# Kernel tuning notes

Hardware: AMD Instinct MI355X
Metric: run time of the kernel (lower is better)

## Reference

```python
import jax, jax.numpy as jnp
import numpy as np

MAX_SEQ_LEN = 64
BEAM = 8
NEG_INF = -1e30


def gru_cell(x, h, W_ih, W_hh, b_ih, b_hh):
    # PyTorch GRUCell math. x: [N,E], h: [N,H]
    H = h.shape[-1]
    gi = x @ W_ih.T + b_ih  # [N,3H]
    gh = h @ W_hh.T + b_hh  # [N,3H]
    r = jax.nn.sigmoid(gi[:, :H] + gh[:, :H])
    z = jax.nn.sigmoid(gi[:, H:2 * H] + gh[:, H:2 * H])
    n = jnp.tanh(gi[:, 2 * H:] + r * gh[:, 2 * H:])
    return (1.0 - z) * n + z * h


def decoder_step(tok, h, embedding, W_ih, W_hh, b_ih, b_hh, W_out, b_out):
    emb = embedding[tok]                      # [N,E] gather
    h2 = gru_cell(emb, h, W_ih, W_hh, b_ih, b_hh)
    logits = h2 @ W_out.T + b_out             # [N,V]
    return logits, h2


def beam_search(encoded, embedding, W_ih, W_hh, b_ih, b_hh, W_out, b_out, bos_index, eos_index):
    B, H = encoded.shape
    V = embedding.shape[0]
    K, T = BEAM, MAX_SEQ_LEN
    dec = lambda tok, h: decoder_step(tok, h, embedding, W_ih, W_hh, b_ih, b_hh, W_out, b_out)

    # step 0: bos
    bos = jnp.full((B,), bos_index, jnp.int32)
    logits0, h0 = dec(bos, encoded)
    lp0 = jax.nn.log_softmax(logits0, axis=1)
    vals, idx = jax.lax.top_k(lp0, K)  # [B,K]
    lp_hist = jnp.zeros((B, K, T), jnp.float32).at[:, :, 0].set(vals)
    tok_hist = jnp.zeros((B, K, T), jnp.int32).at[:, :, 0].set(idx)
    last = idx.reshape(B * K)
    # hidden.repeat(1, K).view(B*K, H): tile each row K times
    hidden = jnp.broadcast_to(h0[:, None, :], (B, K, H)).reshape(B * K, H)
    is_eos = (jnp.arange(V) == eos_index)  # [V]

    def step(carry, t):
        last, hidden, prev_vals, prev_tok, lp_hist, tok_hist = carry
        logits, hidden = dec(last, hidden)
        lp = jax.nn.log_softmax(logits, axis=1).reshape(B, K, V)
        combined = prev_vals[:, :, None] + lp
        has_fin = (prev_tok == eos_index)[:, :, None]  # [B,K,1]
        masked = jnp.where(is_eos[None, None, :] & has_fin, 0.0, combined)
        masked = jnp.where((~is_eos)[None, None, :] & has_fin, NEG_INF, masked)
        vals, idx = jax.lax.top_k(masked.reshape(B, K * V), K)  # [B,K]
        tokens = idx % V
        which = idx // V
        hidden = jnp.take_along_axis(hidden.reshape(B, K, H), which[:, :, None], axis=1).reshape(B * K, H)
        lp_hist = jnp.take_along_axis(lp_hist, which[:, :, None], axis=1)
        tok_hist = jnp.take_along_axis(tok_hist, which[:, :, None], axis=1)
        lp_hist = jax.lax.dynamic_update_slice(lp_hist, vals[:, :, None], (0, 0, t))
        tok_hist = jax.lax.dynamic_update_slice(tok_hist, tokens[:, :, None], (0, 0, t))
        return (tokens.reshape(B * K), hidden, vals, tokens, lp_hist, tok_hist), None

    carry = (last, hidden, vals, idx, lp_hist, tok_hist)
    (last, hidden, vals, idx, lp_hist, tok_hist), _ = jax.lax.scan(step, carry, jnp.arange(1, T))
    return lp_hist, tok_hist


def setup_inputs() -> dict:
    key = jax.random.key(0)
    ks = jax.random.split(key, 8)
    B, V, E, H = 4, 32000, 512, 1024
    s = 0.05
    return {
        "encoded": jax.random.normal(ks[0], (B, H), jnp.float32),
        "embedding": jax.random.normal(ks[1], (V, E), jnp.float32) * s,
        "W_ih": jax.random.normal(ks[2], (3 * H, E), jnp.float32) * s,
        "W_hh": jax.random.normal(ks[3], (3 * H, H), jnp.float32) * s,
        "b_ih": jax.random.normal(ks[4], (3 * H,), jnp.float32) * s,
        "b_hh": jax.random.normal(ks[5], (3 * H,), jnp.float32) * s,
        "W_out": jax.random.normal(ks[6], (V, H), jnp.float32) * s,
        "b_out": jax.random.normal(ks[7], (V,), jnp.float32) * s,
        "bos_index": 1,
        "eos_index": 2,
    }


def reference(encoded, embedding, W_ih, W_hh, b_ih, b_hh, W_out, b_out, bos_index, eos_index):
    return beam_search(encoded, embedding, W_ih, W_hh, b_ih, b_hh, W_out, b_out, bos_index, eos_index)
```

## Files before the change

kernel.cpp:

```cpp
#include <hip/hip_runtime.h>

typedef unsigned long long ull;

#define EMB 512
#define HID 1024
#define NV  32000
#define NB  4
#define NT  64

__device__ __forceinline__ ull umax64(ull a, ull b) { return a > b ? a : b; }
__device__ __forceinline__ ull umin64(ull a, ull b) { return a < b ? a : b; }

__device__ __forceinline__ ull packkey(float v, unsigned idx) {
  unsigned u = __float_as_uint(v);
  u ^= (u >> 31) ? 0xFFFFFFFFu : 0x80000000u;
  return ((ull)u << 32) | (ull)(0xFFFFFFFFu - idx);
}

__global__ void k_prep(const float* __restrict__ encoded, const float* __restrict__ emb,
                       const int* __restrict__ bosp,
                       float* __restrict__ hT, float* __restrict__ embX)
{
  int g = blockIdx.x * 256 + threadIdx.x;
  if (g < 32768) {
    int k = g >> 5, n = g & 31;
    hT[g] = encoded[(n >> 3) * HID + k];
  } else {
    int g2 = g - 32768;
    int k = g2 >> 5;
    embX[g2] = emb[(size_t)(*bosp) * EMB + k];
  }
}

template<int SECK>
__device__ __forceinline__ void gemm_panel(
    const float* __restrict__ Wrow,
    int K,
    int kb0, int nsec,
    const float* __restrict__ xT,
    float* __restrict__ outP)
{
  __shared__ float xlds[SECK * 32];
  __shared__ float wlds[4][2][16 * 64];

  const int t = threadIdx.x;
  const int l = t & 63;
  const int wq = t >> 6;
  const int jg = l & 7;
  const int ng = l >> 3;
  const int lrow = l >> 2;
  const int lk4 = (l & 3) * 4;

  float acc[8][4];
#pragma unroll
  for (int i = 0; i < 8; ++i)
#pragma unroll
    for (int q = 0; q < 4; ++q) acc[i][q] = 0.f;

  for (int sec = 0; sec < nsec; ++sec) {
    const int ks = kb0 + sec * SECK;
    __syncthreads();
    {
      const float* src = xT + (size_t)ks * 32;
      for (int i = t * 4; i < SECK * 32; i += 1024)
        *(float4*)(&xlds[i]) = *(const float4*)(src + i);
    }
    __syncthreads();

    const float* wsrc = Wrow + (size_t)(wq * 64 + lrow) * K + ks + lk4;
    const int nch = SECK / 16;

    float4 wr[4];
#pragma unroll
    for (int p = 0; p < 4; ++p) wr[p] = *(const float4*)(wsrc + (size_t)(p * 16) * K);
#pragma unroll
    for (int p = 0; p < 4; ++p) {
      float* wd = &wlds[wq][0][0];
      wd[(lk4 + 0) * 64 + p * 16 + lrow] = wr[p].x;
      wd[(lk4 + 1) * 64 + p * 16 + lrow] = wr[p].y;
      wd[(lk4 + 2) * 64 + p * 16 + lrow] = wr[p].z;
      wd[(lk4 + 3) * 64 + p * 16 + lrow] = wr[p].w;
    }
    int buf = 0;
    for (int c = 0; c < nch; ++c) {
      if (c + 1 < nch) {
#pragma unroll
        for (int p = 0; p < 4; ++p)
          wr[p] = *(const float4*)(wsrc + (size_t)(p * 16) * K + (c + 1) * 16);
      }
      const float* wb = &wlds[wq][buf][0];
      const float* xb = xlds + (size_t)(c * 16) * 32;
#pragma unroll
      for (int k = 0; k < 16; ++k) {
        float4 w0 = *(const float4*)(wb + k * 64 + jg * 8);
        float4 w1 = *(const float4*)(wb + k * 64 + jg * 8 + 4);
        float4 xv = *(const float4*)(xb + k * 32 + ng * 4);
        acc[0][0] = fmaf(w0.x, xv.x, acc[0][0]); acc[0][1] = fmaf(w0.x, xv.y, acc[0][1]);
        acc[0][2] = fmaf(w0.x, xv.z, acc[0][2]); acc[0][3] = fmaf(w0.x, xv.w, acc[0][3]);
        acc[1][0] = fmaf(w0.y, xv.x, acc[1][0]); acc[1][1] = fmaf(w0.y, xv.y, acc[1][1]);
        acc[1][2] = fmaf(w0.y, xv.z, acc[1][2]); acc[1][3] = fmaf(w0.y, xv.w, acc[1][3]);
        acc[2][0] = fmaf(w0.z, xv.x, acc[2][0]); acc[2][1] = fmaf(w0.z, xv.y, acc[2][1]);
        acc[2][2] = fmaf(w0.z, xv.z, acc[2][2]); acc[2][3] = fmaf(w0.z, xv.w, acc[2][3]);
        acc[3][0] = fmaf(w0.w, xv.x, acc[3][0]); acc[3][1] = fmaf(w0.w, xv.y, acc[3][1]);
        acc[3][2] = fmaf(w0.w, xv.z, acc[3][2]); acc[3][3] = fmaf(w0.w, xv.w, acc[3][3]);
        acc[4][0] = fmaf(w1.x, xv.x, acc[4][0]); acc[4][1] = fmaf(w1.x, xv.y, acc[4][1]);
        acc[4][2] = fmaf(w1.x, xv.z, acc[4][2]); acc[4][3] = fmaf(w1.x, xv.w, acc[4][3]);
        acc[5][0] = fmaf(w1.y, xv.x, acc[5][0]); acc[5][1] = fmaf(w1.y, xv.y, acc[5][1]);
        acc[5][2] = fmaf(w1.y, xv.z, acc[5][2]); acc[5][3] = fmaf(w1.y, xv.w, acc[5][3]);
        acc[6][0] = fmaf(w1.z, xv.x, acc[6][0]); acc[6][1] = fmaf(w1.z, xv.y, acc[6][1]);
        acc[6][2] = fmaf(w1.z, xv.z, acc[6][2]); acc[6][3] = fmaf(w1.z, xv.w, acc[6][3]);
        acc[7][0] = fmaf(w1.w, xv.x, acc[7][0]); acc[7][1] = fmaf(w1.w, xv.y, acc[7][1]);
        acc[7][2] = fmaf(w1.w, xv.z, acc[7][2]); acc[7][3] = fmaf(w1.w, xv.w, acc[7][3]);
      }
      if (c + 1 < nch) {
        float* wd = &wlds[wq][buf ^ 1][0];
#pragma unroll
        for (int p = 0; p < 4; ++p) {
          wd[(lk4 + 0) * 64 + p * 16 + lrow] = wr[p].x;
          wd[(lk4 + 1) * 64 + p * 16 + lrow] = wr[p].y;
          wd[(lk4 + 2) * 64 + p * 16 + lrow] = wr[p].z;
          wd[(lk4 + 3) * 64 + p * 16 + lrow] = wr[p].w;
        }
      }
      buf ^= 1;
    }
  }

#pragma unroll
  for (int i = 0; i < 8; ++i)
    *(float4*)(outP + (size_t)(wq * 64 + jg * 8 + i) * 32 + ng * 4) =
        make_float4(acc[i][0], acc[i][1], acc[i][2], acc[i][3]);
}

__global__ __launch_bounds__(256, 2) void k_gates(
    const float* __restrict__ Wih, const float* __restrict__ Whh,
    const float* __restrict__ embX, const float* __restrict__ hT,
    float* __restrict__ gHp, float* __restrict__ gIp)
{
  const int bx = blockIdx.x;
  if (bx < 96) {
    const int jt = bx % 12, s = bx / 12;
    gemm_panel<128>(Whh + (size_t)jt * 256 * HID, HID, s * 128, 1, hT,
                    gHp + (size_t)s * (3072 * 32) + (size_t)jt * 256 * 32);
  } else {
    const int r = bx - 96;
    const int jt = r % 12, s = r / 12;
    gemm_panel<128>(Wih + (size_t)jt * 256 * EMB, EMB, s * 128, 1, embX,
                    gIp + (size_t)s * (3072 * 32) + (size_t)jt * 256 * 32);
  }
}

__global__ __launch_bounds__(256) void k_combine(
    const float* __restrict__ gHp, const float* __restrict__ gIp,
    const float* __restrict__ bih, const float* __restrict__ bhh,
    const float* __restrict__ hT, float* __restrict__ h2T)
{
  int g = blockIdx.x * 256 + threadIdx.x;
  int n = g & 31, i = g >> 5;
  float gir = bih[i], giz = bih[1024 + i], gin = bih[2048 + i];
#pragma unroll
  for (int s = 0; s < 4; ++s) {
    const float* P = gIp + (size_t)s * (3072 * 32);
    gir += P[(size_t)i * 32 + n];
    giz += P[(size_t)(1024 + i) * 32 + n];
    gin += P[(size_t)(2048 + i) * 32 + n];
  }
  float ghr = bhh[i], ghz = bhh[1024 + i], ghn = bhh[2048 + i];
#pragma unroll
  for (int s = 0; s < 8; ++s) {
    const float* P = gHp + (size_t)s * (3072 * 32);
    ghr += P[(size_t)i * 32 + n];
    ghz += P[(size_t)(1024 + i) * 32 + n];
    ghn += P[(size_t)(2048 + i) * 32 + n];
  }
  float r = 1.f / (1.f + expf(-(gir + ghr)));
  float z = 1.f / (1.f + expf(-(giz + ghz)));
  float nn = tanhf(gin + r * ghn);
  h2T[g] = (1.f - z) * nn + z * hT[g];
}

__global__ __launch_bounds__(256, 2) void k_logits(
    const float* __restrict__ Wout, const float* __restrict__ h2T,
    float* __restrict__ logitsP, int NS)
{
  const int jt = blockIdx.x % 125;
  const int s = blockIdx.x / 125;
  const int KperS = 1024 / NS;
  gemm_panel<256>(Wout + (size_t)jt * 256 * HID, HID, s * KperS, KperS / 256, h2T,
                  logitsP + (size_t)s * (NV * 32) + (size_t)jt * 256 * 32);
}

__global__ __launch_bounds__(256) void k_reduce(
    const float* __restrict__ logitsP, const float* __restrict__ bout,
    float* __restrict__ logitsN, float* __restrict__ lsePart, int NS)
{
  __shared__ float tile[64][33];
  const int t = threadIdx.x;
  const int j0 = blockIdx.x * 64;

  {
    const int n = t & 31;
    const int jb = (t >> 5) * 8;
    float v[8];
#pragma unroll
    for (int i = 0; i < 8; ++i) v[i] = bout[j0 + jb + i];
    for (int s = 0; s < NS; ++s) {
      const float* P = logitsP + (size_t)s * (NV * 32) + (size_t)(j0 + jb) * 32 + n;
#pragma unroll
      for (int i = 0; i < 8; ++i) v[i] += P[(size_t)i * 32];
    }
#pragma unroll
    for (int i = 0; i < 8; ++i) tile[jb + i][n] = v[i];
  }
  __syncthreads();
  {
    const int jl = t & 63;
    const int wq = t >> 6;
#pragma unroll
    for (int q = 0; q < 8; ++q) {
      const int nn = wq * 8 + q;
      float val = tile[jl][nn];
      logitsN[(size_t)nn * NV + j0 + jl] = val;
      float m = val;
      m = fmaxf(m, __shfl_xor(m, 1, 64));
      m = fmaxf(m, __shfl_xor(m, 2, 64));
      m = fmaxf(m, __shfl_xor(m, 4, 64));
      m = fmaxf(m, __shfl_xor(m, 8, 64));
      m = fmaxf(m, __shfl_xor(m, 16, 64));
      m = fmaxf(m, __shfl_xor(m, 32, 64));
      float sx = expf(val - m);
      sx += __shfl_xor(sx, 1, 64);
      sx += __shfl_xor(sx, 2, 64);
      sx += __shfl_xor(sx, 4, 64);
      sx += __shfl_xor(sx, 8, 64);
      sx += __shfl_xor(sx, 16, 64);
      sx += __shfl_xor(sx, 32, 64);
      if (jl == 0) {
        lsePart[(size_t)blockIdx.x * 64 + nn * 2] = m;
        lsePart[(size_t)blockIdx.x * 64 + nn * 2 + 1] = sx;
      }
    }
  }
}

__global__ __launch_bounds__(256) void k_topkA(
    const float* __restrict__ logitsN, const float* __restrict__ lsePart,
    const float* __restrict__ prev_vals, const int* __restrict__ prev_tok,
    const int* __restrict__ eosp, ull* __restrict__ top8A, int mode)
{
  const int t = threadIdx.x;
  const int b = blockIdx.x >> 5;
  const int c = blockIdx.x & 31;

  __shared__ float pm[32][8];
  __shared__ float ps[32][8];
  __shared__ float A[8];
  __shared__ ull wm[4];

  {
    const int n8 = t & 7;
    const int grp = t >> 3;
    float m = -3.0e38f, s = 0.f;
    for (int p = grp; p < 500; p += 32) {
      float2 q = *(const float2*)(lsePart + (size_t)p * 64 + (b * 8 + n8) * 2);
      float Mx = fmaxf(m, q.x);
      s = s * expf(m - Mx) + q.y * expf(q.x - Mx);
      m = Mx;
    }
    pm[grp][n8] = m; ps[grp][n8] = s;
    __syncthreads();
    for (int off2 = 16; off2 >= 1; off2 >>= 1) {
      if (grp < off2) {
        float m1 = pm[grp][n8], s1 = ps[grp][n8];
        float m2 = pm[grp + off2][n8], s2 = ps[grp + off2][n8];
        float Mx = fmaxf(m1, m2);
        pm[grp][n8] = Mx;
        ps[grp][n8] = s1 * expf(m1 - Mx) + s2 * expf(m2 - Mx);
      }
      __syncthreads();
    }
    if (t < 8) A[t] = pm[0][t] + logf(ps[0][t]);
    __syncthreads();
  }

  const int eos = *eosp;

  ull t8[8];
#pragma unroll
  for (int j = 0; j < 8; ++j) t8[j] = 0ULL;

  if (mode == 1) {
    const int kb = c >> 2;
    const int v0 = (c & 3) * 8000;
    const bool fin = (prev_tok[b * 8 + kb] == eos);
    const float add = prev_vals[b * 8 + kb] - A[kb];
    const float* row = logitsN + (size_t)(b * 8 + kb) * NV;
    for (int v = v0 + t; v < v0 + 8000; v += 256) {
      float val;
      if (fin) val = (v == eos) ? 0.f : -1e30f;
      else val = row[v] + add;
      ull key = packkey(val, (unsigned)(kb * NV + v));
      if (key > t8[7]) {
        t8[7] = key;
#pragma unroll
        for (int q = 7; q >= 1; --q) {
          ull hi = umax64(t8[q - 1], t8[q]);
          ull lo = umin64(t8[q - 1], t8[q]);
          t8[q - 1] = hi; t8[q] = lo;
        }
      }
    }
  } else {
    const int v0 = c * 1000;
    const float add = -A[0];
    const float* row = logitsN + (size_t)(b * 8) * NV;
    for (int v = v0 + t; v < v0 + 1000; v += 256) {
      float val = row[v] + add;
      ull key = packkey(val, (unsigned)v);
      if (key > t8[7]) {
        t8[7] = key;
#pragma unroll
        for (int q = 7; q >= 1; --q) {
          ull hi = umax64(t8[q - 1], t8[q]);
          ull lo = umin64(t8[q - 1], t8[q]);
          t8[q - 1] = hi; t8[q] = lo;
        }
      }
    }
  }

  int pi = 0;
  for (int r = 0; r < 8; ++r) {
    ull cand = (pi < 8) ? t8[pi] : 0ULL;
#pragma unroll
    for (int off = 1; off < 64; off <<= 1) cand = umax64(cand, __shfl_xor(cand, off, 64));
    if ((t & 63) == 0) wm[t >> 6] = cand;
    __syncthreads();
    ull win = umax64(umax64(wm[0], wm[1]), umax64(wm[2], wm[3]));
    if (pi < 8 && t8[pi] == win) ++pi;
    if (t == 0) top8A[((size_t)b * 32 + c) * 8 + r] = win;
    __syncthreads();
  }
}

__global__ __launch_bounds__(256) void k_topkB(
    const ull* __restrict__ top8A,
    float* __restrict__ prev_vals, int* __restrict__ prev_tok,
    const float* __restrict__ lp_src, float* __restrict__ lp_dst,
    const int* __restrict__ tok_src, int* __restrict__ tok_dst,
    const float* __restrict__ h2T, float* __restrict__ hT,
    const float* __restrict__ emb, float* __restrict__ embX,
    int step, int mode)
{
  const int t = threadIdx.x;
  const int b = blockIdx.x;
  __shared__ ull wm[4];
  __shared__ float vals8[8];
  __shared__ int tok8[8];
  __shared__ int which8[8];

  ull mykey = top8A[(size_t)b * 256 + t];
  int done = 0;
  for (int r = 0; r < 8; ++r) {
    ull cand = done ? 0ULL : mykey;
#pragma unroll
    for (int off = 1; off < 64; off <<= 1) cand = umax64(cand, __shfl_xor(cand, off, 64));
    if ((t & 63) == 0) wm[t >> 6] = cand;
    __syncthreads();
    ull win = umax64(umax64(wm[0], wm[1]), umax64(wm[2], wm[3]));
    if (!done && mykey == win) done = 1;
    if (t == 0) {
      unsigned idx = 0xFFFFFFFFu - (unsigned)(win & 0xFFFFFFFFull);
      unsigned u = (unsigned)(win >> 32);
      u = (u >> 31) ? (u ^ 0x80000000u) : ~u;
      vals8[r] = __uint_as_float(u);
      if (mode == 1) { tok8[r] = (int)(idx % NV); which8[r] = (int)(idx / NV); }
      else { tok8[r] = (int)idx; which8[r] = r; }
    }
    __syncthreads();
  }

  if (t < 8) {
    prev_vals[b * 8 + t] = vals8[t];
    prev_tok[b * 8 + t] = tok8[t];
  }
  for (int idx = t; idx < 512; idx += 256) {
    int j = idx >> 6;
    int tt = idx & 63;
    float lv; int tv;
    if (tt == step) { lv = vals8[j]; tv = tok8[j]; }
    else if (mode == 0) { lv = 0.f; tv = 0; }
    else {
      int w = which8[j];
      lv = lp_src[b * 512 + w * 64 + tt];
      tv = tok_src[b * 512 + w * 64 + tt];
    }
    lp_dst[b * 512 + idx] = lv;
    tok_dst[b * 512 + idx] = tv;
  }
  for (int idx = t; idx < 8192; idx += 256) {
    int kk = idx >> 3;
    int j = idx & 7;
    hT[kk * 32 + b * 8 + j] = h2T[kk * 32 + b * 8 + which8[j]];
  }
  {
    int j = t >> 5;
    int kbase = (t & 31) * 16;
    const float* src = emb + (size_t)tok8[j] * EMB + kbase;
#pragma unroll
    for (int q = 0; q < 4; ++q) {
      float4 v = *(const float4*)(src + 4 * q);
      embX[(kbase + 4 * q + 0) * 32 + b * 8 + j] = v.x;
      embX[(kbase + 4 * q + 1) * 32 + b * 8 + j] = v.y;
      embX[(kbase + 4 * q + 2) * 32 + b * 8 + j] = v.z;
      embX[(kbase + 4 * q + 3) * 32 + b * 8 + j] = v.w;
    }
  }
}

__global__ void k_final(const float* __restrict__ lp_hist, const int* __restrict__ tok_hist,
                        float* __restrict__ out)
{
  int g = blockIdx.x * 256 + threadIdx.x;
  if (g < 2048) out[g] = lp_hist[g];
  else out[g] = (float)tok_hist[g - 2048];
}

extern "C" void kernel_launch(void* const* d_in, const int* in_sizes, int n_in,
                              void* d_out, int out_size, void* d_ws, size_t ws_size,
                              hipStream_t stream)
{
  (void)in_sizes; (void)n_in; (void)out_size;
  const float* encoded   = (const float*)d_in[0];
  const float* embedding = (const float*)d_in[1];
  const float* Wih       = (const float*)d_in[2];
  const float* Whh       = (const float*)d_in[3];
  const float* bih       = (const float*)d_in[4];
  const float* bhh       = (const float*)d_in[5];
  const float* Wout      = (const float*)d_in[6];
  const float* bout      = (const float*)d_in[7];
  const int*   bosp      = (const int*)d_in[8];
  const int*   eosp      = (const int*)d_in[9];

  char* p = (char*)d_ws;
  size_t off = 0;
  auto ALLOC = [&](size_t bytes) -> void* {
    void* r = p + off;
    off += (bytes + 255) & ~(size_t)255;
    return r;
  };
  float* hT        = (float*)ALLOC((size_t)HID * 32 * 4);
  float* h2T       = (float*)ALLOC((size_t)HID * 32 * 4);
  float* embX      = (float*)ALLOC((size_t)EMB * 32 * 4);
  float* gHp       = (float*)ALLOC((size_t)8 * 3072 * 32 * 4);
  float* gIp       = (float*)ALLOC((size_t)4 * 3072 * 32 * 4);
  float* logitsN   = gHp;
  float* lsePart   = (float*)ALLOC((size_t)500 * 64 * 4);
  ull*   top8A     = (ull*)ALLOC((size_t)NB * 32 * 8 * 8);
  float* prev_vals = (float*)ALLOC(32 * 4);
  int*   prev_tok  = (int*)ALLOC(32 * 4);
  float* lp0       = (float*)ALLOC(2048 * 4);
  float* lp1       = (float*)ALLOC(2048 * 4);
  int*   tok0      = (int*)ALLOC(2048 * 4);
  int*   tok1      = (int*)ALLOC(2048 * 4);

  int NS = 4;
  if (off + (size_t)4 * NV * 32 * 4 > ws_size) NS = 2;
  if (off + (size_t)2 * NV * 32 * 4 > ws_size) NS = 1;
  float* logitsP = (float*)ALLOC((size_t)NS * NV * 32 * 4);

  k_prep<<<192, 256, 0, stream>>>(encoded, embedding, bosp, hT, embX);
  for (int t = 0; t < NT; ++t) {
    k_gates<<<144, 256, 0, stream>>>(Wih, Whh, embX, hT, gHp, gIp);
    k_combine<<<128, 256, 0, stream>>>(gHp, gIp, bih, bhh, hT, h2T);
    k_logits<<<125 * NS, 256, 0, stream>>>(Wout, h2T, logitsP, NS);
    k_reduce<<<500, 256, 0, stream>>>(logitsP, bout, logitsN, lsePart, NS);
    const int mode = (t == 0) ? 0 : 1;
    k_topkA<<<128, 256, 0, stream>>>(logitsN, lsePart, prev_vals, prev_tok, eosp, top8A, mode);
    float* lps = (t & 1) ? lp0 : lp1;
    float* lpd = (t & 1) ? lp1 : lp0;
    int*   tks = (t & 1) ? tok0 : tok1;
    int*   tkd = (t & 1) ? tok1 : tok0;
    k_topkB<<<NB, 256, 0, stream>>>(top8A, prev_vals, prev_tok, lps, lpd, tks, tkd,
                                    h2T, hT, embedding, embX, t, mode);
  }
  k_final<<<16, 256, 0, stream>>>(lp1, tok1, (float*)d_out);
}
```

Baseline: 6.897 ms.

## Fuse beam-search step kernels into one persistent cooperative megakernel with grid barriers

Replaces the per-step sequence of six kernel launches (64 steps, hundreds of launches) with a single cooperative persistent kernel that loops over steps and separates phases with a custom hierarchical atomic grid barrier. It also changes the logits GEMM section size from 256 to 128 k-rows. The aim is to remove launch overhead and inter-kernel gaps. In exchange each phase now has a grid-wide barrier, and small phases such as topkB run on only a few blocks while the rest of the grid spins. The old multi-launch path is kept as a fallback if the cooperative launch fails.

```diff
diff --git a/kernel.cpp b/kernel.cpp
--- a/kernel.cpp
+++ b/kernel.cpp
@@ -17,32 +17,46 @@
   return ((ull)u << 32) | (ull)(0xFFFFFFFFu - idx);
 }
 
-__global__ void k_prep(const float* __restrict__ encoded, const float* __restrict__ emb,
-                       const int* __restrict__ bosp,
-                       float* __restrict__ hT, float* __restrict__ embX)
-{
-  int g = blockIdx.x * 256 + threadIdx.x;
-  if (g < 32768) {
-    int k = g >> 5, n = g & 31;
-    hT[g] = encoded[(n >> 3) * HID + k];
-  } else {
-    int g2 = g - 32768;
-    int k = g2 >> 5;
-    embX[g2] = emb[(size_t)(*bosp) * EMB + k];
-  }
+struct GridBar { unsigned cnt[8 * 32]; unsigned mid[32]; unsigned gen[32]; };
+
+__device__ __forceinline__ void gridbar(GridBar* gb, int W) {
+  __syncthreads();
+  if (threadIdx.x == 0) {
+    __threadfence();
+    const int lane = (int)(blockIdx.x & 7);
+    const int rem = W & 7;
+    const unsigned nlane = (unsigned)((W >> 3) + (lane < rem ? 1 : 0));
+    const unsigned nlanes = (unsigned)(W < 8 ? W : 8);
+    unsigned g = __hip_atomic_load(&gb->gen[0], __ATOMIC_RELAXED, __HIP_MEMORY_SCOPE_AGENT);
+    unsigned a = __hip_atomic_fetch_add(&gb->cnt[lane * 32], 1u, __ATOMIC_RELAXED,
+                                        __HIP_MEMORY_SCOPE_AGENT);
+    if (a == nlane - 1u) {
+      __hip_atomic_store(&gb->cnt[lane * 32], 0u, __ATOMIC_RELAXED, __HIP_MEMORY_SCOPE_AGENT);
+      unsigned m = __hip_atomic_fetch_add(&gb->mid[0], 1u, __ATOMIC_RELAXED,
+                                          __HIP_MEMORY_SCOPE_AGENT);
+      if (m == nlanes - 1u) {
+        __hip_atomic_store(&gb->mid[0], 0u, __ATOMIC_RELAXED, __HIP_MEMORY_SCOPE_AGENT);
+        __hip_atomic_store(&gb->gen[0], g + 1u, __ATOMIC_RELEASE, __HIP_MEMORY_SCOPE_AGENT);
+      }
+    }
+    while (__hip_atomic_load(&gb->gen[0], __ATOMIC_RELAXED, __HIP_MEMORY_SCOPE_AGENT) == g)
+      __builtin_amdgcn_s_sleep(2);
+    __threadfence();
+  }
+  __syncthreads();
+}
+
+__global__ void k_zero(unsigned* w) {
+  if (threadIdx.x < sizeof(GridBar) / 4) w[threadIdx.x] = 0;
 }
 
 template<int SECK>
-__device__ __forceinline__ void gemm_panel(
-    const float* __restrict__ Wrow,
-    int K,
-    int kb0, int nsec,
-    const float* __restrict__ xT,
-    float* __restrict__ outP)
-{
-  __shared__ float xlds[SECK * 32];
-  __shared__ float wlds[4][2][16 * 64];
-
+__device__ __forceinline__ void gemm_panel_m(
+    float* __restrict__ xlds,
+    float (* __restrict__ wlds)[2][1024],
+    const float* __restrict__ Wrow, int K, int kb0, int nsec,
+    const float* __restrict__ xT, float* __restrict__ outP)
+{
   const int t = threadIdx.x;
   const int l = t & 63;
   const int wq = t >> 6;
@@ -132,30 +146,11 @@
         make_float4(acc[i][0], acc[i][1], acc[i][2], acc[i][3]);
 }
 
-__global__ __launch_bounds__(256, 2) void k_gates(
-    const float* __restrict__ Wih, const float* __restrict__ Whh,
-    const float* __restrict__ embX, const float* __restrict__ hT,
-    float* __restrict__ gHp, float* __restrict__ gIp)
-{
-  const int bx = blockIdx.x;
-  if (bx < 96) {
-    const int jt = bx % 12, s = bx / 12;
-    gemm_panel<128>(Whh + (size_t)jt * 256 * HID, HID, s * 128, 1, hT,
-                    gHp + (size_t)s * (3072 * 32) + (size_t)jt * 256 * 32);
-  } else {
-    const int r = bx - 96;
-    const int jt = r % 12, s = r / 12;
-    gemm_panel<128>(Wih + (size_t)jt * 256 * EMB, EMB, s * 128, 1, embX,
-                    gIp + (size_t)s * (3072 * 32) + (size_t)jt * 256 * 32);
-  }
-}
-
-__global__ __launch_bounds__(256) void k_combine(
-    const float* __restrict__ gHp, const float* __restrict__ gIp,
+__device__ __forceinline__ void combine_one(
+    int g, const float* __restrict__ gHp, const float* __restrict__ gIp,
     const float* __restrict__ bih, const float* __restrict__ bhh,
     const float* __restrict__ hT, float* __restrict__ h2T)
 {
-  int g = blockIdx.x * 256 + threadIdx.x;
   int n = g & 31, i = g >> 5;
   float gir = bih[i], giz = bih[1024 + i], gin = bih[2048 + i];
 #pragma unroll
@@ -179,24 +174,13 @@
   h2T[g] = (1.f - z) * nn + z * hT[g];
 }
 
-__global__ __launch_bounds__(256, 2) void k_logits(
-    const float* __restrict__ Wout, const float* __restrict__ h2T,
-    float* __restrict__ logitsP, int NS)
-{
-  const int jt = blockIdx.x % 125;
-  const int s = blockIdx.x / 125;
-  const int KperS = 1024 / NS;
-  gemm_panel<256>(Wout + (size_t)jt * 256 * HID, HID, s * KperS, KperS / 256, h2T,
-                  logitsP + (size_t)s * (NV * 32) + (size_t)jt * 256 * 32);
-}
-
-__global__ __launch_bounds__(256) void k_reduce(
+__device__ __forceinline__ void reduce_one(
+    int bx, float (* __restrict__ tile)[33],
     const float* __restrict__ logitsP, const float* __restrict__ bout,
     float* __restrict__ logitsN, float* __restrict__ lsePart, int NS)
 {
-  __shared__ float tile[64][33];
   const int t = threadIdx.x;
-  const int j0 = blockIdx.x * 64;
+  const int j0 = bx * 64;
 
   {
     const int n = t & 31;
@@ -236,26 +220,22 @@
       sx += __shfl_xor(sx, 16, 64);
       sx += __shfl_xor(sx, 32, 64);
       if (jl == 0) {
-        lsePart[(size_t)blockIdx.x * 64 + nn * 2] = m;
-        lsePart[(size_t)blockIdx.x * 64 + nn * 2 + 1] = sx;
-      }
-    }
-  }
-}
-
-__global__ __launch_bounds__(256) void k_topkA(
+        lsePart[(size_t)bx * 64 + nn * 2] = m;
+        lsePart[(size_t)bx * 64 + nn * 2 + 1] = sx;
+      }
+    }
+  }
+}
+
+struct TAsh { float pm[32][8]; float ps[32][8]; float A[8]; ull wm[4]; };
+
+__device__ __forceinline__ void topkA_one(
+    int b, int c, TAsh* S,
     const float* __restrict__ logitsN, const float* __restrict__ lsePart,
     const float* __restrict__ prev_vals, const int* __restrict__ prev_tok,
-    const int* __restrict__ eosp, ull* __restrict__ top8A, int mode)
+    int eos, ull* __restrict__ top8A, int mode)
 {
   const int t = threadIdx.x;
-  const int b = blockIdx.x >> 5;
-  const int c = blockIdx.x & 31;
-
-  __shared__ float pm[32][8];
-  __shared__ float ps[32][8];
-  __shared__ float A[8];
-  __shared__ ull wm[4];
 
   {
     const int n8 = t & 7;
@@ -267,23 +247,21 @@
       s = s * expf(m - Mx) + q.y * expf(q.x - Mx);
       m = Mx;
     }
-    pm[grp][n8] = m; ps[grp][n8] = s;
+    S->pm[grp][n8] = m; S->ps[grp][n8] = s;
     __syncthreads();
     for (int off2 = 16; off2 >= 1; off2 >>= 1) {
       if (grp < off2) {
-        float m1 = pm[grp][n8], s1 = ps[grp][n8];
-        float m2 = pm[grp + off2][n8], s2 = ps[grp + off2][n8];
+        float m1 = S->pm[grp][n8], s1 = S->ps[grp][n8];
+        float m2 = S->pm[grp + off2][n8], s2 = S->ps[grp + off2][n8];
         float Mx = fmaxf(m1, m2);
-        pm[grp][n8] = Mx;
-        ps[grp][n8] = s1 * expf(m1 - Mx) + s2 * expf(m2 - Mx);
+        S->pm[grp][n8] = Mx;
+        S->ps[grp][n8] = s1 * expf(m1 - Mx) + s2 * expf(m2 - Mx);
       }
       __syncthreads();
     }
-    if (t < 8) A[t] = pm[0][t] + logf(ps[0][t]);
-    __syncthreads();
-  }
-
-  const int eos = *eosp;
+    if (t < 8) S->A[t] = S->pm[0][t] + logf(S->ps[0][t]);
+    __syncthreads();
+  }
 
   ull t8[8];
 #pragma unroll
@@ -293,7 +271,7 @@
     const int kb = c >> 2;
     const int v0 = (c & 3) * 8000;
     const bool fin = (prev_tok[b * 8 + kb] == eos);
-    const float add = prev_vals[b * 8 + kb] - A[kb];
+    const float add = prev_vals[b * 8 + kb] - S->A[kb];
     const float* row = logitsN + (size_t)(b * 8 + kb) * NV;
     for (int v = v0 + t; v < v0 + 8000; v += 256) {
       float val;
@@ -312,7 +290,7 @@
     }
   } else {
     const int v0 = c * 1000;
-    const float add = -A[0];
+    const float add = -S->A[0];
     const float* row = logitsN + (size_t)(b * 8) * NV;
     for (int v = v0 + t; v < v0 + 1000; v += 256) {
       float val = row[v] + add;
@@ -334,13 +312,259 @@
     ull cand = (pi < 8) ? t8[pi] : 0ULL;
 #pragma unroll
     for (int off = 1; off < 64; off <<= 1) cand = umax64(cand, __shfl_xor(cand, off, 64));
-    if ((t & 63) == 0) wm[t >> 6] = cand;
-    __syncthreads();
-    ull win = umax64(umax64(wm[0], wm[1]), umax64(wm[2], wm[3]));
+    if ((t & 63) == 0) S->wm[t >> 6] = cand;
+    __syncthreads();
+    ull win = umax64(umax64(S->wm[0], S->wm[1]), umax64(S->wm[2], S->wm[3]));
     if (pi < 8 && t8[pi] == win) ++pi;
     if (t == 0) top8A[((size_t)b * 32 + c) * 8 + r] = win;
     __syncthreads();
   }
+}
+
+struct TBsh { ull wm[4]; float vals8[8]; int tok8[8]; int which8[8]; };
+
+__device__ __forceinline__ void topkB_one(
+    int b, TBsh* S, const ull* __restrict__ top8A,
+    float* __restrict__ prev_vals, int* __restrict__ prev_tok,
+    const float* __restrict__ lp_src, float* __restrict__ lp_dst,
+    const int* __restrict__ tok_src, int* __restrict__ tok_dst,
+    const float* __restrict__ h2T, float* __restrict__ hT,
+    const float* __restrict__ emb, float* __restrict__ embX,
+    int step, int mode)
+{
+  const int t = threadIdx.x;
+
+  ull mykey = top8A[(size_t)b * 256 + t];
+  int done = 0;
+  for (int r = 0; r < 8; ++r) {
+    ull cand = done ? 0ULL : mykey;
+#pragma unroll
+    for (int off = 1; off < 64; off <<= 1) cand = umax64(cand, __shfl_xor(cand, off, 64));
+    if ((t & 63) == 0) S->wm[t >> 6] = cand;
+    __syncthreads();
+    ull win = umax64(umax64(S->wm[0], S->wm[1]), umax64(S->wm[2], S->wm[3]));
+    if (!done && mykey == win) done = 1;
+    if (t == 0) {
+      unsigned idx = 0xFFFFFFFFu - (unsigned)(win & 0xFFFFFFFFull);
+      unsigned u = (unsigned)(win >> 32);
+      u = (u >> 31) ? (u ^ 0x80000000u) : ~u;
+      S->vals8[r] = __uint_as_float(u);
+      if (mode == 1) { S->tok8[r] = (int)(idx % NV); S->which8[r] = (int)(idx / NV); }
+      else { S->tok8[r] = (int)idx; S->which8[r] = r; }
+    }
+    __syncthreads();
+  }
+
+  if (t < 8) {
+    prev_vals[b * 8 + t] = S->vals8[t];
+    prev_tok[b * 8 + t] = S->tok8[t];
+  }
+  for (int idx = t; idx < 512; idx += 256) {
+    int j = idx >> 6;
+    int tt = idx & 63;
+    float lv; int tv;
+    if (tt == step) { lv = S->vals8[j]; tv = S->tok8[j]; }
+    else if (mode == 0) { lv = 0.f; tv = 0; }
+    else {
+      int w = S->which8[j];
+      lv = lp_src[b * 512 + w * 64 + tt];
+      tv = tok_src[b * 512 + w * 64 + tt];
+    }
+    lp_dst[b * 512 + idx] = lv;
+    tok_dst[b * 512 + idx] = tv;
+  }
+  for (int idx = t; idx < 8192; idx += 256) {
+    int kk = idx >> 3;
+    int j = idx & 7;
+    hT[kk * 32 + b * 8 + j] = h2T[kk * 32 + b * 8 + S->which8[j]];
+  }
+  {
+    int j = t >> 5;
+    int kbase = (t & 31) * 16;
+    const float* src = emb + (size_t)S->tok8[j] * EMB + kbase;
+#pragma unroll
+    for (int q = 0; q < 4; ++q) {
+      float4 v = *(const float4*)(src + 4 * q);
+      embX[(kbase + 4 * q + 0) * 32 + b * 8 + j] = v.x;
+      embX[(kbase + 4 * q + 1) * 32 + b * 8 + j] = v.y;
+      embX[(kbase + 4 * q + 2) * 32 + b * 8 + j] = v.z;
+      embX[(kbase + 4 * q + 3) * 32 + b * 8 + j] = v.w;
+    }
+  }
+}
+
+union MegaLDS {
+  struct { float x[128 * 32]; float w[4][2][1024]; } gp;
+  float tile[64][33];
+  TAsh ta;
+  TBsh tb;
+};
+
+struct MegaArgs {
+  const float* encoded; const float* embedding;
+  const float* Wih; const float* Whh; const float* bih; const float* bhh;
+  const float* Wout; const float* bout;
+  const int* bosp; const int* eosp;
+  float* hT; float* h2T; float* embX; float* gHp; float* gIp;
+  float* logitsN; float* lsePart; ull* top8A;
+  float* prev_vals; int* prev_tok;
+  float* lp0; float* lp1; int* tok0; int* tok1;
+  float* logitsP; int NS;
+  GridBar* gb; float* outp;
+};
+
+__global__ __launch_bounds__(256, 2) void k_mega(MegaArgs a)
+{
+  __shared__ MegaLDS L;
+  const int W = (int)gridDim.x;
+  const int bid = (int)blockIdx.x;
+  const int t = (int)threadIdx.x;
+  const int KperS = 1024 / a.NS;
+  const int NPANL = 125 * a.NS;
+
+  for (int g = bid * 256 + t; g < 49152; g += W * 256) {
+    if (g < 32768) {
+      int k = g >> 5, n = g & 31;
+      a.hT[g] = a.encoded[(n >> 3) * HID + k];
+    } else {
+      int g2 = g - 32768;
+      int k = g2 >> 5;
+      a.embX[g2] = a.embedding[(size_t)(*a.bosp) * EMB + k];
+    }
+  }
+  gridbar(a.gb, W);
+  const int eos = *a.eosp;
+
+  for (int st = 0; st < NT; ++st) {
+    for (int p = bid; p < 144; p += W) {
+      if (p < 96) {
+        int jt = p % 12, s = p / 12;
+        gemm_panel_m<128>(L.gp.x, L.gp.w, a.Whh + (size_t)jt * 256 * HID, HID, s * 128, 1,
+                          a.hT, a.gHp + (size_t)s * (3072 * 32) + (size_t)jt * 256 * 32);
+      } else {
+        int r = p - 96, jt = r % 12, s = r / 12;
+        gemm_panel_m<128>(L.gp.x, L.gp.w, a.Wih + (size_t)jt * 256 * EMB, EMB, s * 128, 1,
+                          a.embX, a.gIp + (size_t)s * (3072 * 32) + (size_t)jt * 256 * 32);
+      }
+    }
+    gridbar(a.gb, W);
+
+    for (int g = bid * 256 + t; g < 32768; g += W * 256)
+      combine_one(g, a.gHp, a.gIp, a.bih, a.bhh, a.hT, a.h2T);
+    gridbar(a.gb, W);
+
+    for (int p = bid; p < NPANL; p += W) {
+      int jt = p % 125, s = p / 125;
+      gemm_panel_m<128>(L.gp.x, L.gp.w, a.Wout + (size_t)jt * 256 * HID, HID, s * KperS,
+                        KperS / 128, a.h2T,
+                        a.logitsP + (size_t)s * (NV * 32) + (size_t)jt * 256 * 32);
+    }
+    gridbar(a.gb, W);
+
+    for (int c = bid; c < 500; c += W) {
+      reduce_one(c, L.tile, a.logitsP, a.bout, a.logitsN, a.lsePart, a.NS);
+      __syncthreads();
+    }
+    gridbar(a.gb, W);
+
+    const int mode = (st == 0) ? 0 : 1;
+
+    for (int it = bid; it < 128; it += W)
+      topkA_one(it >> 5, it & 31, &L.ta, a.logitsN, a.lsePart, a.prev_vals, a.prev_tok,
+                eos, a.top8A, mode);
+    gridbar(a.gb, W);
+
+    {
+      float* lps = (st & 1) ? a.lp0 : a.lp1;
+      float* lpd = (st & 1) ? a.lp1 : a.lp0;
+      int* tks = (st & 1) ? a.tok0 : a.tok1;
+      int* tkd = (st & 1) ? a.tok1 : a.tok0;
+      for (int b = bid; b < NB; b += W)
+        topkB_one(b, &L.tb, a.top8A, a.prev_vals, a.prev_tok, lps, lpd, tks, tkd,
+                  a.h2T, a.hT, a.embedding, a.embX, st, mode);
+    }
+    gridbar(a.gb, W);
+  }
+
+  for (int g = bid * 256 + t; g < 4096; g += W * 256) {
+    if (g < 2048) a.outp[g] = a.lp1[g];
+    else a.outp[g] = (float)a.tok1[g - 2048];
+  }
+}
+
+__global__ void k_prep(const float* __restrict__ encoded, const float* __restrict__ emb,
+                       const int* __restrict__ bosp,
+                       float* __restrict__ hT, float* __restrict__ embX)
+{
+  int g = blockIdx.x * 256 + threadIdx.x;
+  if (g < 32768) {
+    int k = g >> 5, n = g & 31;
+    hT[g] = encoded[(n >> 3) * HID + k];
+  } else {
+    int g2 = g - 32768;
+    int k = g2 >> 5;
+    embX[g2] = emb[(size_t)(*bosp) * EMB + k];
+  }
+}
+
+__global__ __launch_bounds__(256, 2) void k_gates(
+    const float* __restrict__ Wih, const float* __restrict__ Whh,
+    const float* __restrict__ embX, const float* __restrict__ hT,
+    float* __restrict__ gHp, float* __restrict__ gIp)
+{
+  __shared__ float xlds[128 * 32];
+  __shared__ float wlds[4][2][1024];
+  const int bx = blockIdx.x;
+  if (bx < 96) {
+    const int jt = bx % 12, s = bx / 12;
+    gemm_panel_m<128>(xlds, wlds, Whh + (size_t)jt * 256 * HID, HID, s * 128, 1, hT,
+                      gHp + (size_t)s * (3072 * 32) + (size_t)jt * 256 * 32);
+  } else {
+    const int r = bx - 96;
+    const int jt = r % 12, s = r / 12;
+    gemm_panel_m<128>(xlds, wlds, Wih + (size_t)jt * 256 * EMB, EMB, s * 128, 1, embX,
+                      gIp + (size_t)s * (3072 * 32) + (size_t)jt * 256 * 32);
+  }
+}
+
+__global__ __launch_bounds__(256) void k_combine(
+    const float* __restrict__ gHp, const float* __restrict__ gIp,
+    const float* __restrict__ bih, const float* __restrict__ bhh,
+    const float* __restrict__ hT, float* __restrict__ h2T)
+{
+  int g = blockIdx.x * 256 + threadIdx.x;
+  combine_one(g, gHp, gIp, bih, bhh, hT, h2T);
+}
+
+__global__ __launch_bounds__(256, 2) void k_logits(
+    const float* __restrict__ Wout, const float* __restrict__ h2T,
+    float* __restrict__ logitsP, int NS)
+{
+  __shared__ float xlds[128 * 32];
+  __shared__ float wlds[4][2][1024];
+  const int jt = blockIdx.x % 125;
+  const int s = blockIdx.x / 125;
+  const int KperS = 1024 / NS;
+  gemm_panel_m<128>(xlds, wlds, Wout + (size_t)jt * 256 * HID, HID, s * KperS, KperS / 128,
+                    h2T, logitsP + (size_t)s * (NV * 32) + (size_t)jt * 256 * 32);
+}
+
+__global__ __launch_bounds__(256) void k_reduce(
+    const float* __restrict__ logitsP, const float* __restrict__ bout,
+    float* __restrict__ logitsN, float* __restrict__ lsePart, int NS)
+{
+  __shared__ float tile[64][33];
+  reduce_one(blockIdx.x, tile, logitsP, bout, logitsN, lsePart, NS);
+}
+
+__global__ __launch_bounds__(256) void k_topkA(
+    const float* __restrict__ logitsN, const float* __restrict__ lsePart,
+    const float* __restrict__ prev_vals, const int* __restrict__ prev_tok,
+    const int* __restrict__ eosp, ull* __restrict__ top8A, int mode)
+{
+  __shared__ TAsh S;
+  topkA_one(blockIdx.x >> 5, blockIdx.x & 31, &S, logitsN, lsePart, prev_vals, prev_tok,
+            *eosp, top8A, mode);
 }
 
 __global__ __launch_bounds__(256) void k_topkB(
@@ -352,70 +576,9 @@
     const float* __restrict__ emb, float* __restrict__ embX,
     int step, int mode)
 {
-  const int t = threadIdx.x;
-  const int b = blockIdx.x;
-  __shared__ ull wm[4];
-  __shared__ float vals8[8];
-  __shared__ int tok8[8];
-  __shared__ int which8[8];
-
-  ull mykey = top8A[(size_t)b * 256 + t];
-  int done = 0;
-  for (int r = 0; r < 8; ++r) {
-    ull cand = done ? 0ULL : mykey;
-#pragma unroll
-    for (int off = 1; off < 64; off <<= 1) cand = umax64(cand, __shfl_xor(cand, off, 64));
-    if ((t & 63) == 0) wm[t >> 6] = cand;
-    __syncthreads();
-    ull win = umax64(umax64(wm[0], wm[1]), umax64(wm[2], wm[3]));
-    if (!done && mykey == win) done = 1;
-    if (t == 0) {
-      unsigned idx = 0xFFFFFFFFu - (unsigned)(win & 0xFFFFFFFFull);
-      unsigned u = (unsigned)(win >> 32);
-      u = (u >> 31) ? (u ^ 0x80000000u) : ~u;
-      vals8[r] = __uint_as_float(u);
-      if (mode == 1) { tok8[r] = (int)(idx % NV); which8[r] = (int)(idx / NV); }
-      else { tok8[r] = (int)idx; which8[r] = r; }
-    }
-    __syncthreads();
-  }
-
-  if (t < 8) {
-    prev_vals[b * 8 + t] = vals8[t];
-    prev_tok[b * 8 + t] = tok8[t];
-  }
-  for (int idx = t; idx < 512; idx += 256) {
-    int j = idx >> 6;
-    int tt = idx & 63;
-    float lv; int tv;
-    if (tt == step) { lv = vals8[j]; tv = tok8[j]; }
-    else if (mode == 0) { lv = 0.f; tv = 0; }
-    else {
-      int w = which8[j];
-      lv = lp_src[b * 512 + w * 64 + tt];
-      tv = tok_src[b * 512 + w * 64 + tt];
-    }
-    lp_dst[b * 512 + idx] = lv;
-    tok_dst[b * 512 + idx] = tv;
-  }
-  for (int idx = t; idx < 8192; idx += 256) {
-    int kk = idx >> 3;
-    int j = idx & 7;
-    hT[kk * 32 + b * 8 + j] = h2T[kk * 32 + b * 8 + which8[j]];
-  }
-  {
-    int j = t >> 5;
-    int kbase = (t & 31) * 16;
-    const float* src = emb + (size_t)tok8[j] * EMB + kbase;
-#pragma unroll
-    for (int q = 0; q < 4; ++q) {
-      float4 v = *(const float4*)(src + 4 * q);
-      embX[(kbase + 4 * q + 0) * 32 + b * 8 + j] = v.x;
-      embX[(kbase + 4 * q + 1) * 32 + b * 8 + j] = v.y;
-      embX[(kbase + 4 * q + 2) * 32 + b * 8 + j] = v.z;
-      embX[(kbase + 4 * q + 3) * 32 + b * 8 + j] = v.w;
-    }
-  }
+  __shared__ TBsh S;
+  topkB_one(blockIdx.x, &S, top8A, prev_vals, prev_tok, lp_src, lp_dst, tok_src, tok_dst,
+            h2T, hT, emb, embX, step, mode);
 }
 
 __global__ void k_final(const float* __restrict__ lp_hist, const int* __restrict__ tok_hist,
@@ -463,11 +626,34 @@
   float* lp1       = (float*)ALLOC(2048 * 4);
   int*   tok0      = (int*)ALLOC(2048 * 4);
   int*   tok1      = (int*)ALLOC(2048 * 4);
+  GridBar* gb      = (GridBar*)ALLOC(sizeof(GridBar));
 
   int NS = 4;
   if (off + (size_t)4 * NV * 32 * 4 > ws_size) NS = 2;
   if (off + (size_t)2 * NV * 32 * 4 > ws_size) NS = 1;
   float* logitsP = (float*)ALLOC((size_t)NS * NV * 32 * 4);
+
+  k_zero<<<1, 512, 0, stream>>>((unsigned*)gb);
+
+  MegaArgs ma;
+  ma.encoded = encoded; ma.embedding = embedding;
+  ma.Wih = Wih; ma.Whh = Whh; ma.bih = bih; ma.bhh = bhh;
+  ma.Wout = Wout; ma.bout = bout; ma.bosp = bosp; ma.eosp = eosp;
+  ma.hT = hT; ma.h2T = h2T; ma.embX = embX; ma.gHp = gHp; ma.gIp = gIp;
+  ma.logitsN = logitsN; ma.lsePart = lsePart; ma.top8A = top8A;
+  ma.prev_vals = prev_vals; ma.prev_tok = prev_tok;
+  ma.lp0 = lp0; ma.lp1 = lp1; ma.tok0 = tok0; ma.tok1 = tok1;
+  ma.logitsP = logitsP; ma.NS = NS; ma.gb = gb; ma.outp = (float*)d_out;
+
+  int occ = 0;
+  if (hipOccupancyMaxActiveBlocksPerMultiprocessor(&occ, k_mega, 256, 0) != hipSuccess ||
+      occ < 1) occ = 1;
+  int W = (occ >= 2) ? 500 : 250;
+
+  void* kargs[] = { &ma };
+  hipError_t e = hipLaunchCooperativeKernel(k_mega, dim3(W), dim3(256), kargs, 0, stream);
+  if (e == hipSuccess) return;
+  (void)hipGetLastError();
 
   k_prep<<<192, 256, 0, stream>>>(encoded, embedding, bosp, hT, embX);
   for (int t = 0; t < NT; ++t) {
```

After: 11.87 ms. 1.72x slower.
